# Optimization experiments

Measured on AMD Instinct MI355X. Metric: run time of the kernel, lower is better.

The kernel has to match this reference:

```python
import jax, jax.numpy as jnp
import numpy as np

M = 12          # persons per frame
K = 2           # partition channels from conv1da (1024 = 2*512)
D = 512         # GCN channel dim / LSTM hidden
C_IN = 4096     # backbone feature dim
NUM_CLASSES = 8


def setup_inputs() -> dict:
    key = jax.random.key(0)
    ks = jax.random.split(key, 8)
    N, T = 16, 32
    NT = N * T
    base_out = jax.random.normal(ks[0], (NT, M, C_IN), dtype=jnp.float32)
    dist = jax.random.uniform(ks[1], (N, T, 3, K, M, M), dtype=jnp.float32)
    # conv1da: Conv1d(4096 -> 1024, k=1, bias=False) == matmul with [1024, 4096]
    w_a = jax.random.normal(ks[2], (K * D, C_IN), dtype=jnp.float32) * 0.02
    # LSTM(512, 512, 1): torch gate order i, f, g, o
    s = 1.0 / np.sqrt(D)
    w_ih = jax.random.uniform(ks[3], (4 * D, D), minval=-s, maxval=s, dtype=jnp.float32)
    w_hh = jax.random.uniform(ks[4], (4 * D, D), minval=-s, maxval=s, dtype=jnp.float32)
    b_ih = jax.random.uniform(ks[5], (4 * D,), minval=-s, maxval=s, dtype=jnp.float32)
    b_hh = jax.random.uniform(ks[6], (4 * D,), minval=-s, maxval=s, dtype=jnp.float32)
    # gclassifier: Linear(512 -> num_classes)
    w_cls = jax.random.normal(ks[7], (NUM_CLASSES, D), dtype=jnp.float32) * 0.01
    b_cls = jnp.zeros((NUM_CLASSES,), dtype=jnp.float32)
    return {"base_out": base_out, "dist": dist, "w_a": w_a,
            "w_ih": w_ih, "w_hh": w_hh, "b_ih": b_ih, "b_hh": b_hh,
            "w_cls": w_cls, "b_cls": b_cls, "n_videos": N}


def reference(base_out, dist, w_a, w_ih, w_hh, b_ih, b_hh, w_cls, b_cls, n_videos):
    NT = base_out.shape[0]
    N = n_videos
    T = NT // N
    # conv1da (1x1 conv, no bias): [NT, M, 4096] -> [NT, K*D, M] -> [NT, K, D, M]
    node1 = jnp.einsum('nmc,oc->nom', base_out, w_a).reshape(NT, K, D, M)
    # fused three-way adjacency aggregation: node1a + node1b + node1c
    A = (dist[:, :, 2] + dist[:, :, 1] + dist[:, :, 0]).reshape(NT, K, M, M)
    node = jnp.einsum('nkcv,nkvw->ncw', node1, A)  # [NT, D, M]
    node = jax.nn.relu(node)
    # AdaptiveAvgPool1d(1) over the M persons
    pooled = node.mean(axis=2)                      # [NT, D]
    seq = pooled.reshape(N, T, D)
    # torch nn.LSTM default batch_first=False: iterates over axis 0 (N), batch=T
    def step(carry, x_t):
        h, c = carry
        g = x_t @ w_ih.T + b_ih + h @ w_hh.T + b_hh  # [T, 4D]
        i, f, gg, o = jnp.split(g, 4, axis=-1)
        c = jax.nn.sigmoid(f) * c + jax.nn.sigmoid(i) * jnp.tanh(gg)
        h = jax.nn.sigmoid(o) * jnp.tanh(c)
        return (h, c), h
    h0 = jnp.zeros((T, D), dtype=seq.dtype)
    c0 = jnp.zeros((T, D), dtype=seq.dtype)
    _, hs = jax.lax.scan(step, (h0, c0), seq)       # [N, T, D]
    last = hs[:, -1, :]                              # video_feat[:, -1, :]
    return last @ w_cls.T + b_cls                    # [N, num_classes]
```

## Files before the change

kernel.cpp:

```cpp
#include <hip/hip_runtime.h>
#include <math.h>

#define MM 12
#define KK 2
#define DD 512
#define CIN 4096
#define NCLS 8
#define NV 16
#define TT 32

typedef unsigned long long u64;

#define PART_F   0
#define POOLED_F 786432
#define GX_F     794624
#define SLOT_F   827392

__global__ __launch_bounds__(256) void k_gemm(const float* __restrict__ w_a,
                                              const float* __restrict__ base_out,
                                              float* __restrict__ part) {
    const int ks = blockIdx.x;
    const int ot = blockIdx.y;
    const int jt = blockIdx.z;
    const int tid = threadIdx.x;

    __shared__ __align__(16) float As[16][68];
    __shared__ __align__(16) float Bs[16][68];

    const int to = tid & 15;
    const int tj = tid >> 4;

    const int lrow = tid >> 2;
    const int lq   = tid & 3;
    const size_t a_base = (size_t)(ot * 64 + lrow) * CIN;
    const int j_stage = jt * 64 + lrow;
    const int n_stage = j_stage / 12;
    const int m_stage = j_stage - n_stage * 12;
    const size_t b_base = (size_t)((n_stage * TT + 31) * MM + m_stage) * CIN;

    float acc[4][4];
#pragma unroll
    for (int i = 0; i < 4; ++i)
#pragma unroll
        for (int jj = 0; jj < 4; ++jj) acc[i][jj] = 0.f;

    int cc0 = ks * 1024;
    for (int it = 0; it < 64; ++it, cc0 += 16) {
        float4 av = *(const float4*)&w_a[a_base + cc0 + lq * 4];
        float4 bv = *(const float4*)&base_out[b_base + cc0 + lq * 4];
        __syncthreads();
        As[lq * 4 + 0][lrow] = av.x; As[lq * 4 + 1][lrow] = av.y;
        As[lq * 4 + 2][lrow] = av.z; As[lq * 4 + 3][lrow] = av.w;
        Bs[lq * 4 + 0][lrow] = bv.x; Bs[lq * 4 + 1][lrow] = bv.y;
        Bs[lq * 4 + 2][lrow] = bv.z; Bs[lq * 4 + 3][lrow] = bv.w;
        __syncthreads();
#pragma unroll
        for (int cl = 0; cl < 16; ++cl) {
            float4 a = *(const float4*)&As[cl][to * 4];
            float4 b = *(const float4*)&Bs[cl][tj * 4];
            acc[0][0] += a.x * b.x; acc[0][1] += a.x * b.y; acc[0][2] += a.x * b.z; acc[0][3] += a.x * b.w;
            acc[1][0] += a.y * b.x; acc[1][1] += a.y * b.y; acc[1][2] += a.y * b.z; acc[1][3] += a.y * b.w;
            acc[2][0] += a.z * b.x; acc[2][1] += a.z * b.y; acc[2][2] += a.z * b.z; acc[2][3] += a.z * b.w;
            acc[3][0] += a.w * b.x; acc[3][1] += a.w * b.y; acc[3][2] += a.w * b.z; acc[3][3] += a.w * b.w;
        }
    }

    const int o_base = ot * 64 + to * 4;
#pragma unroll
    for (int jj = 0; jj < 4; ++jj) {
        const int j = jt * 64 + tj * 4 + jj;
        float4 v = make_float4(acc[0][jj], acc[1][jj], acc[2][jj], acc[3][jj]);
        *(float4*)&part[(size_t)ks * (192 * 1024) + (size_t)j * 1024 + o_base] = v;
    }
}

__global__ __launch_bounds__(256) void k_pool(const float* __restrict__ part,
                                              const float* __restrict__ dist,
                                              float* __restrict__ pooled) {
    const int n = blockIdx.x;
    const int tid = threadIdx.x;
    __shared__ float Asum[KK][MM][MM];

    const size_t dbase = (size_t)(n * TT + 31) * (3 * KK * MM * MM);
    for (int f = tid; f < KK * MM * MM; f += 256) {
        const int k = f / (MM * MM);
        const int rem = f - k * (MM * MM);
        float s = dist[dbase + 0 * (KK * MM * MM) + k * (MM * MM) + rem]
                + dist[dbase + 1 * (KK * MM * MM) + k * (MM * MM) + rem]
                + dist[dbase + 2 * (KK * MM * MM) + k * (MM * MM) + rem];
        Asum[k][rem / MM][rem % MM] = s;
    }
    __syncthreads();

    for (int c = tid; c < DD; c += 256) {
        float nd[KK][MM];
#pragma unroll
        for (int k = 0; k < KK; ++k)
#pragma unroll
            for (int v = 0; v < MM; ++v) {
                const size_t off = (size_t)(n * MM + v) * 1024 + (k * DD + c);
                nd[k][v] = part[off] + part[off + 1 * (192 * 1024)]
                         + part[off + 2 * (192 * 1024)] + part[off + 3 * (192 * 1024)];
            }
        float accm = 0.f;
#pragma unroll
        for (int w = 0; w < MM; ++w) {
            float sw = 0.f;
#pragma unroll
            for (int k = 0; k < KK; ++k)
#pragma unroll
                for (int v = 0; v < MM; ++v) sw += nd[k][v] * Asum[k][v][w];
            accm += fmaxf(sw, 0.f);
        }
        pooled[n * DD + c] = accm * (1.f / 12.f);
    }
}

__global__ __launch_bounds__(256) void k_gx(const float* __restrict__ pooled,
                                            const float* __restrict__ w_ih,
                                            const float* __restrict__ b_ih,
                                            const float* __restrict__ b_hh,
                                            float* __restrict__ gx) {
    const int wg = blockIdx.x;
    const int tid = threadIdx.x;
    __shared__ __align__(16) float w_s[16][516];

    for (int f = tid; f < 16 * DD; f += 256) {
        const int r = f >> 9, col = f & 511;
        w_s[r][col] = w_ih[(size_t)(wg * 16 + r) * DD + col];
    }
    __syncthreads();

    const int r = tid & 15;
    const int n = tid >> 4;
    const float4* wr = (const float4*)&w_s[r][0];
    const float4* pv = (const float4*)(pooled + n * DD);
    float acc = 0.f;
#pragma unroll 8
    for (int q = 0; q < DD / 4; ++q) {
        float4 a = wr[q], b = pv[q];
        acc += a.x * b.x + a.y * b.y + a.z * b.z + a.w * b.w;
    }
    const int row = wg * 16 + r;
    gx[n * (4 * DD) + row] = acc + b_ih[row] + b_hh[row];
}

__global__ __launch_bounds__(256) void k_lstm(const float* __restrict__ w_hh,
                                              const float* __restrict__ gx,
                                              const float* __restrict__ w_cls,
                                              const float* __restrict__ b_cls,
                                              u64* __restrict__ slots,
                                              float* __restrict__ out) {
    const int wg = blockIdx.x;
    const int tid = threadIdx.x;

    __shared__ __align__(16) float whh_s[16][516];
    __shared__ __align__(16) float h_s[DD];
    __shared__ float dot_s[16];

    for (int f = tid; f < 16 * DD; f += 256) {
        const int rl = f >> 9, col = f & 511;
        const int gate = rl >> 2, dl = rl & 3;
        whh_s[rl][col] = w_hh[(size_t)(gate * DD + wg * 4 + dl) * DD + col];
    }

    float c_reg = 0.f;
    const int rl = tid >> 4;
    const int lj = tid & 15;

    for (int s = 0; s < NV; ++s) {
        if (s == 0) {
            for (int d = tid; d < DD; d += 256) h_s[d] = 0.f;
        } else {
            const u64* slot = slots + (size_t)(s - 1) * DD;
            for (int d = tid; d < DD; d += 256) {
                u64 v;
                do {
                    v = __hip_atomic_load(&slot[d], __ATOMIC_RELAXED, __HIP_MEMORY_SCOPE_AGENT);
                } while ((unsigned)(v & 0xffffffffull) != (unsigned)s);
                union { unsigned u; float f; } cv; cv.u = (unsigned)(v >> 32);
                h_s[d] = cv.f;
            }
        }
        __syncthreads();

        float p = 0.f;
        const float4* wrow = (const float4*)&whh_s[rl][0];
        const float4* hv4 = (const float4*)h_s;
#pragma unroll
        for (int q = 0; q < 8; ++q) {
            float4 wv = wrow[lj + 16 * q];
            float4 hv = hv4[lj + 16 * q];
            p += wv.x * hv.x + wv.y * hv.y + wv.z * hv.z + wv.w * hv.w;
        }
#pragma unroll
        for (int off = 8; off; off >>= 1) p += __shfl_down(p, off, 16);
        if (lj == 0) dot_s[rl] = p;
        __syncthreads();

        if (tid < 4) {
            const int dg = wg * 4 + tid;
            const float* gxs = gx + s * (4 * DD);
            const float pi = gxs[0 * DD + dg] + dot_s[0 + tid];
            const float pf = gxs[1 * DD + dg] + dot_s[4 + tid];
            const float pg = gxs[2 * DD + dg] + dot_s[8 + tid];
            const float po = gxs[3 * DD + dg] + dot_s[12 + tid];
            const float si = 1.f / (1.f + expf(-pi));
            const float sf = 1.f / (1.f + expf(-pf));
            const float so = 1.f / (1.f + expf(-po));
            c_reg = sf * c_reg + si * tanhf(pg);
            const float hn = so * tanhf(c_reg);
            union { float f; unsigned u; } hv_; hv_.f = hn;
            const u64 pack = ((u64)hv_.u << 32) | (u64)(unsigned)(s + 1);
            __hip_atomic_store(&slots[(size_t)s * DD + dg], pack,
                               __ATOMIC_RELAXED, __HIP_MEMORY_SCOPE_AGENT);
        }
    }

    if (wg == 0) {
        __syncthreads();
        for (int f = tid; f < NV * DD; f += 256) {
            const int ss = f >> 9, d = f & 511;
            u64 v;
            do {
                v = __hip_atomic_load(&slots[(size_t)ss * DD + d],
                                      __ATOMIC_RELAXED, __HIP_MEMORY_SCOPE_AGENT);
            } while ((unsigned)(v & 0xffffffffull) != (unsigned)(ss + 1));
            union { unsigned u; float f; } cv; cv.u = (unsigned)(v >> 32);
            whh_s[ss][d] = cv.f;
        }
        __syncthreads();
        if (tid < NV * NCLS) {
            const int n = tid >> 3, cl = tid & 7;
            const float4* hv = (const float4*)&whh_s[n][0];
            const float4* wv = (const float4*)(w_cls + (size_t)cl * DD);
            float acc = b_cls[cl];
#pragma unroll 8
            for (int q = 0; q < DD / 4; ++q) {
                float4 a = hv[q], b = wv[q];
                acc += a.x * b.x + a.y * b.y + a.z * b.z + a.w * b.w;
            }
            out[tid] = acc;
        }
    }
}

extern "C" void kernel_launch(void* const* d_in, const int* in_sizes, int n_in,
                              void* d_out, int out_size, void* d_ws, size_t ws_size,
                              hipStream_t stream) {
    const float* base_out = (const float*)d_in[0];
    const float* dist     = (const float*)d_in[1];
    const float* w_a      = (const float*)d_in[2];
    const float* w_ih     = (const float*)d_in[3];
    const float* w_hh     = (const float*)d_in[4];
    const float* b_ih     = (const float*)d_in[5];
    const float* b_hh     = (const float*)d_in[6];
    const float* w_cls    = (const float*)d_in[7];
    const float* b_cls    = (const float*)d_in[8];
    float* out = (float*)d_out;

    float* ws = (float*)d_ws;
    float* part   = ws + PART_F;
    float* pooled = ws + POOLED_F;
    float* gx     = ws + GX_F;
    u64*   slots  = (u64*)(ws + SLOT_F);

    k_gemm<<<dim3(4, 16, 3), 256, 0, stream>>>(w_a, base_out, part);
    k_pool<<<dim3(16), 256, 0, stream>>>(part, dist, pooled);
    k_gx<<<dim3(128), 256, 0, stream>>>(pooled, w_ih, b_ih, b_hh, gx);
    k_lstm<<<dim3(128), 256, 0, stream>>>(w_hh, gx, w_cls, b_cls, slots, out);
}
```

Baseline: 286.5 us.

## Retile GEMM columns with register prefetch and consolidate LSTM into fewer blocks

The GEMM now tiles 48 columns per block instead of 64, giving 256 blocks rather than 192 for better CU coverage, and prefetches the next K-slice into registers while the current tile is computed. The LSTM now runs 32 workgroups that each own 16 hidden units instead of 128 owning 4. This cuts the number of blocks polling the cross-block step flags, and each block loads W_hh into LDS with float4 copies. Spin loops gain s_sleep backoff to reduce memory pressure from polling, at the cost of longer per-step dot products and possible wake-up latency.

```diff
diff --git a/kernel.cpp b/kernel.cpp
--- a/kernel.cpp
+++ b/kernel.cpp
@@ -25,50 +25,63 @@
     const int tid = threadIdx.x;
 
     __shared__ __align__(16) float As[16][68];
-    __shared__ __align__(16) float Bs[16][68];
+    __shared__ __align__(16) float Bs[16][52];
 
     const int to = tid & 15;
     const int tj = tid >> 4;
 
-    const int lrow = tid >> 2;
-    const int lq   = tid & 3;
-    const size_t a_base = (size_t)(ot * 64 + lrow) * CIN;
-    const int j_stage = jt * 64 + lrow;
+    const int arow = tid >> 2;
+    const int aq   = tid & 3;
+    const size_t a_base = (size_t)(ot * 64 + arow) * CIN;
+
+    const int brow = tid >> 2;
+    const int j_stage = jt * 48 + brow;
     const int n_stage = j_stage / 12;
     const int m_stage = j_stage - n_stage * 12;
     const size_t b_base = (size_t)((n_stage * TT + 31) * MM + m_stage) * CIN;
 
-    float acc[4][4];
+    float acc[4][3];
 #pragma unroll
     for (int i = 0; i < 4; ++i)
 #pragma unroll
-        for (int jj = 0; jj < 4; ++jj) acc[i][jj] = 0.f;
+        for (int jj = 0; jj < 3; ++jj) acc[i][jj] = 0.f;
 
     int cc0 = ks * 1024;
-    for (int it = 0; it < 64; ++it, cc0 += 16) {
-        float4 av = *(const float4*)&w_a[a_base + cc0 + lq * 4];
-        float4 bv = *(const float4*)&base_out[b_base + cc0 + lq * 4];
-        __syncthreads();
-        As[lq * 4 + 0][lrow] = av.x; As[lq * 4 + 1][lrow] = av.y;
-        As[lq * 4 + 2][lrow] = av.z; As[lq * 4 + 3][lrow] = av.w;
-        Bs[lq * 4 + 0][lrow] = bv.x; Bs[lq * 4 + 1][lrow] = bv.y;
-        Bs[lq * 4 + 2][lrow] = bv.z; Bs[lq * 4 + 3][lrow] = bv.w;
-        __syncthreads();
+    float4 av = *(const float4*)&w_a[a_base + cc0 + aq * 4];
+    float4 bv;
+    if (tid < 192) bv = *(const float4*)&base_out[b_base + cc0 + aq * 4];
+
+    for (int it = 0; it < 64; ++it) {
+        __syncthreads();
+        As[aq * 4 + 0][arow] = av.x; As[aq * 4 + 1][arow] = av.y;
+        As[aq * 4 + 2][arow] = av.z; As[aq * 4 + 3][arow] = av.w;
+        if (tid < 192) {
+            Bs[aq * 4 + 0][brow] = bv.x; Bs[aq * 4 + 1][brow] = bv.y;
+            Bs[aq * 4 + 2][brow] = bv.z; Bs[aq * 4 + 3][brow] = bv.w;
+        }
+        __syncthreads();
+        if (it < 63) {
+            cc0 += 16;
+            av = *(const float4*)&w_a[a_base + cc0 + aq * 4];
+            if (tid < 192) bv = *(const float4*)&base_out[b_base + cc0 + aq * 4];
+        }
 #pragma unroll
         for (int cl = 0; cl < 16; ++cl) {
             float4 a = *(const float4*)&As[cl][to * 4];
-            float4 b = *(const float4*)&Bs[cl][tj * 4];
-            acc[0][0] += a.x * b.x; acc[0][1] += a.x * b.y; acc[0][2] += a.x * b.z; acc[0][3] += a.x * b.w;
-            acc[1][0] += a.y * b.x; acc[1][1] += a.y * b.y; acc[1][2] += a.y * b.z; acc[1][3] += a.y * b.w;
-            acc[2][0] += a.z * b.x; acc[2][1] += a.z * b.y; acc[2][2] += a.z * b.z; acc[2][3] += a.z * b.w;
-            acc[3][0] += a.w * b.x; acc[3][1] += a.w * b.y; acc[3][2] += a.w * b.z; acc[3][3] += a.w * b.w;
+            float b0 = Bs[cl][tj];
+            float b1 = Bs[cl][tj + 16];
+            float b2 = Bs[cl][tj + 32];
+            acc[0][0] += a.x * b0; acc[0][1] += a.x * b1; acc[0][2] += a.x * b2;
+            acc[1][0] += a.y * b0; acc[1][1] += a.y * b1; acc[1][2] += a.y * b2;
+            acc[2][0] += a.z * b0; acc[2][1] += a.z * b1; acc[2][2] += a.z * b2;
+            acc[3][0] += a.w * b0; acc[3][1] += a.w * b1; acc[3][2] += a.w * b2;
         }
     }
 
     const int o_base = ot * 64 + to * 4;
 #pragma unroll
-    for (int jj = 0; jj < 4; ++jj) {
-        const int j = jt * 64 + tj * 4 + jj;
+    for (int jj = 0; jj < 3; ++jj) {
+        const int j = jt * 48 + tj + 16 * jj;
         float4 v = make_float4(acc[0][jj], acc[1][jj], acc[2][jj], acc[3][jj]);
         *(float4*)&part[(size_t)ks * (192 * 1024) + (size_t)j * 1024 + o_base] = v;
     }
@@ -154,19 +167,20 @@
     const int wg = blockIdx.x;
     const int tid = threadIdx.x;
 
-    __shared__ __align__(16) float whh_s[16][516];
+    __shared__ __align__(16) float whh_s[64][516];
     __shared__ __align__(16) float h_s[DD];
-    __shared__ float dot_s[16];
-
-    for (int f = tid; f < 16 * DD; f += 256) {
-        const int rl = f >> 9, col = f & 511;
-        const int gate = rl >> 2, dl = rl & 3;
-        whh_s[rl][col] = w_hh[(size_t)(gate * DD + wg * 4 + dl) * DD + col];
+    __shared__ float dot_s[64];
+
+    for (int f = tid; f < 64 * 128; f += 256) {
+        const int rl = f >> 7, q = f & 127;
+        const int gate = rl >> 4, dl = rl & 15;
+        float4 v = *(const float4*)&w_hh[(size_t)(gate * DD + wg * 16 + dl) * DD + q * 4];
+        *(float4*)&whh_s[rl][q * 4] = v;
     }
 
     float c_reg = 0.f;
-    const int rl = tid >> 4;
-    const int lj = tid & 15;
+    const int r  = tid >> 2;
+    const int lp = tid & 3;
 
     for (int s = 0; s < NV; ++s) {
         if (s == 0) {
@@ -174,10 +188,11 @@
         } else {
             const u64* slot = slots + (size_t)(s - 1) * DD;
             for (int d = tid; d < DD; d += 256) {
-                u64 v;
-                do {
+                u64 v = __hip_atomic_load(&slot[d], __ATOMIC_RELAXED, __HIP_MEMORY_SCOPE_AGENT);
+                while ((unsigned)(v & 0xffffffffull) != (unsigned)s) {
+                    __builtin_amdgcn_s_sleep(1);
                     v = __hip_atomic_load(&slot[d], __ATOMIC_RELAXED, __HIP_MEMORY_SCOPE_AGENT);
-                } while ((unsigned)(v & 0xffffffffull) != (unsigned)s);
+                }
                 union { unsigned u; float f; } cv; cv.u = (unsigned)(v >> 32);
                 h_s[d] = cv.f;
             }
@@ -185,26 +200,26 @@
         __syncthreads();
 
         float p = 0.f;
-        const float4* wrow = (const float4*)&whh_s[rl][0];
+        const float4* wrow = (const float4*)&whh_s[r][0];
         const float4* hv4 = (const float4*)h_s;
 #pragma unroll
-        for (int q = 0; q < 8; ++q) {
-            float4 wv = wrow[lj + 16 * q];
-            float4 hv = hv4[lj + 16 * q];
+        for (int q = 0; q < 32; ++q) {
+            float4 wv = wrow[lp + 4 * q];
+            float4 hv = hv4[lp + 4 * q];
             p += wv.x * hv.x + wv.y * hv.y + wv.z * hv.z + wv.w * hv.w;
         }
-#pragma unroll
-        for (int off = 8; off; off >>= 1) p += __shfl_down(p, off, 16);
-        if (lj == 0) dot_s[rl] = p;
-        __syncthreads();
-
-        if (tid < 4) {
-            const int dg = wg * 4 + tid;
+        p += __shfl_down(p, 2, 4);
+        p += __shfl_down(p, 1, 4);
+        if (lp == 0) dot_s[r] = p;
+        __syncthreads();
+
+        if (tid < 16) {
+            const int dg = wg * 16 + tid;
             const float* gxs = gx + s * (4 * DD);
-            const float pi = gxs[0 * DD + dg] + dot_s[0 + tid];
-            const float pf = gxs[1 * DD + dg] + dot_s[4 + tid];
-            const float pg = gxs[2 * DD + dg] + dot_s[8 + tid];
-            const float po = gxs[3 * DD + dg] + dot_s[12 + tid];
+            const float pi = gxs[0 * DD + dg] + dot_s[0  + tid];
+            const float pf = gxs[1 * DD + dg] + dot_s[16 + tid];
+            const float pg = gxs[2 * DD + dg] + dot_s[32 + tid];
+            const float po = gxs[3 * DD + dg] + dot_s[48 + tid];
             const float si = 1.f / (1.f + expf(-pi));
             const float sf = 1.f / (1.f + expf(-pf));
             const float so = 1.f / (1.f + expf(-po));
@@ -218,14 +233,15 @@
     }
 
     if (wg == 0) {
-        __syncthreads();
         for (int f = tid; f < NV * DD; f += 256) {
             const int ss = f >> 9, d = f & 511;
-            u64 v;
-            do {
+            u64 v = __hip_atomic_load(&slots[(size_t)ss * DD + d],
+                                      __ATOMIC_RELAXED, __HIP_MEMORY_SCOPE_AGENT);
+            while ((unsigned)(v & 0xffffffffull) != (unsigned)(ss + 1)) {
+                __builtin_amdgcn_s_sleep(1);
                 v = __hip_atomic_load(&slots[(size_t)ss * DD + d],
                                       __ATOMIC_RELAXED, __HIP_MEMORY_SCOPE_AGENT);
-            } while ((unsigned)(v & 0xffffffffull) != (unsigned)(ss + 1));
+            }
             union { unsigned u; float f; } cv; cv.u = (unsigned)(v >> 32);
             whh_s[ss][d] = cv.f;
         }
@@ -265,8 +281,8 @@
     float* gx     = ws + GX_F;
     u64*   slots  = (u64*)(ws + SLOT_F);
 
-    k_gemm<<<dim3(4, 16, 3), 256, 0, stream>>>(w_a, base_out, part);
+    k_gemm<<<dim3(4, 16, 4), 256, 0, stream>>>(w_a, base_out, part);
     k_pool<<<dim3(16), 256, 0, stream>>>(part, dist, pooled);
     k_gx<<<dim3(128), 256, 0, stream>>>(pooled, w_ih, b_ih, b_hh, gx);
-    k_lstm<<<dim3(128), 256, 0, stream>>>(w_hh, gx, w_cls, b_cls, slots, out);
-}
+    k_lstm<<<dim3(32), 256, 0, stream>>>(w_hh, gx, w_cls, b_cls, slots, out);
+}
```

Measured after the change: 292.0 us. About the same (+1.9%).
